# Optimization experiments

Hardware: AMD Instinct MI355X
Metric: run time of the kernel (lower is better)

Reference implementation:

```python
import jax, jax.numpy as jnp
import numpy as np

EPS = 1e-5
B, N, K = 8, 4096, 20
C_FEAT = 64            # feature channels (C_in)
HEADS, DIM_K, DIM_V = 8, 32, 16   # C_out=128 -> dim_v = 128//8
CH = 64                # ch_raise
C_CAT = 2 * C_FEAT + DIM_V        # 144, concat channel dim
C_OUT = HEADS * DIM_V


def setup_inputs() -> dict:
    key = jax.random.key(0)
    ks = jax.random.split(key, 8)
    s = lambda k, shape: jax.random.normal(k, shape, jnp.float32) * 0.05
    return {
        "x": jax.random.normal(ks[0], (B, N, 3 + C_FEAT), jnp.float32),
        "W1": s(ks[1], (CH, C_CAT)), "g1": jnp.ones(CH), "b1": jnp.zeros(CH),
        "W2": s(ks[2], (CH, CH)),    "g2": jnp.ones(CH), "b2": jnp.zeros(CH),
        "Wv": s(ks[3], (DIM_V, C_CAT)), "gv": jnp.ones(DIM_V), "bv": jnp.zeros(DIM_V),
        "Wk": s(ks[4], (DIM_K, C_CAT)),
        "Wq": s(ks[5], (HEADS * DIM_K, CH)), "gq": jnp.ones(HEADS * DIM_K), "bq": jnp.zeros(HEADS * DIM_K),
        "Wh": s(ks[6], (DIM_V, 3)),
    }


def _bn(t, g, b):
    # BatchNorm (train-mode batch stats, biased var) over all axes but channel (last)
    axes = tuple(range(t.ndim - 1))
    mu = t.mean(axes, keepdims=True)
    var = t.var(axes, keepdims=True)
    return (t - mu) * jax.lax.rsqrt(var + EPS) * g + b


def reference(x, W1, g1, b1, W2, g2, b2, Wv, gv, bv, Wk, Wq, gq, bq, Wh):
    xyz = x[..., :3]                         # [B,N,3]
    feat = x[..., 3:]                        # [B,N,C_FEAT]
    # KNN via squared distances (same formula as square_distance)
    sq = jnp.sum(xyz * xyz, -1)              # [B,N]
    d = sq[:, :, None] + sq[:, None, :] - 2.0 * jnp.einsum('bnc,bmc->bnm', xyz, xyz)
    _, idx = jax.lax.top_k(-d, K)            # smallest K -> [B,N,K]
    bi = jnp.arange(B)[:, None, None]
    nb_xyz = xyz[bi, idx]                    # [B,N,K,3]
    nb_feat = feat[bi, idx]                  # [B,N,K,C_FEAT]
    gpn = nb_feat - feat[:, :, None, :]      # grouped_points_norm
    rel = nb_xyz - xyz[:, :, None, :]        # relative positions
    pos = jnp.einsum('vc,bnkc->bnkv', Wh, rel)   # mlp_h (1x1 conv)
    fcat = jnp.concatenate(
        [gpn, jnp.broadcast_to(feat[:, :, None, :], (B, N, K, C_FEAT)), pos], -1)  # [B,N,K,C_CAT]
    # mlp: two 1x1 conv + BN + ReLU, then max over K
    h = jax.nn.relu(_bn(jnp.einsum('oc,bnkc->bnko', W1, fcat), g1, b1))
    h = jax.nn.relu(_bn(jnp.einsum('oc,bnkc->bnko', W2, h), g2, b2))
    fq = h.max(2)                            # [B,N,CH]
    q = jax.nn.relu(_bn(jnp.einsum('oc,bnc->bno', Wq, fq), gq, bq))   # [B,N,H*DK]
    q = q.reshape(B, N, HEADS, DIM_K).transpose(0, 2, 3, 1)           # b h d n
    v = _bn(jnp.einsum('vc,bnkc->bnkv', Wv, fcat), gv, bv)            # [B,N,K,DIM_V]
    kk = jax.nn.softmax(jnp.einsum('dc,bnkc->bnkd', Wk, fcat), axis=2)  # softmax over K
    kv = jnp.einsum('bnkd,bnkv->bdvn', kk, v)                         # [B,DK,DV,N]
    out = jnp.einsum('bhdn,bdvn->bhvn', q, kv)                        # [B,H,DV,N]
    out = out.reshape(B, C_OUT, N)                                    # b (h v) n
    return (xyz, out)
```

## Files before the change

### kernel.cpp

```cpp
#include <hip/hip_runtime.h>
#include <hip/hip_bf16.h>

#define NB 8
#define NN 4096
#define KK 20
#define CFEAT 64
#define CCAT 144
#define CHN 64
#define NHEAD 8
#define DKK 32
#define DVV 16
#define NQC 256
#define EPSV 1e-5f
#define BNTOT (NB*NN)
#define ITEMS (BNTOT*KK)

typedef unsigned short ushort_t;
typedef __attribute__((ext_vector_type(8))) short bf16x8;
typedef __attribute__((ext_vector_type(4))) float f32x4;


__device__ __forceinline__ float wred(float v) {
#pragma unroll
  for (int off = 32; off > 0; off >>= 1) v += __shfl_down(v, off);
  return v;
}

__device__ __forceinline__ ushort_t f2bf(float f) {
  unsigned u = __float_as_uint(f);
  return (ushort_t)((u + 0x7fffu + ((u >> 16) & 1u)) >> 16);
}
__device__ __forceinline__ float bf2f(ushort_t h) {
  return __uint_as_float(((unsigned)h) << 16);
}

__device__ __forceinline__ float pdist(float4 me, float4 p) {
  float dot = fmaf(me.x, p.x, fmaf(me.y, p.y, me.z * p.z));
  return fmaf(-2.f, dot, me.w + p.w);
}

__device__ __forceinline__ void insert20(float* bd, float d) {
#pragma unroll
  for (int j = KK - 1; j >= 1; --j)
    bd[j] = __builtin_amdgcn_fmed3f(d, bd[j - 1], bd[j]);
  bd[0] = fminf(bd[0], d);
}

__device__ __forceinline__ void build_chunk(int ch,
    const float* __restrict__ fme, const float* __restrict__ fnb,
    float rx, float ry, float rz, const float* __restrict__ Wh, float* fc)
{
  if (ch < 4) {
    int c0 = ch * 16;
#pragma unroll
    for (int j = 0; j < 16; j += 4) {
      float4 a = *(const float4*)(fnb + c0 + j);
      float4 m = *(const float4*)(fme + c0 + j);
      fc[j + 0] = a.x - m.x; fc[j + 1] = a.y - m.y;
      fc[j + 2] = a.z - m.z; fc[j + 3] = a.w - m.w;
    }
  } else if (ch < 8) {
    int c0 = (ch - 4) * 16;
#pragma unroll
    for (int j = 0; j < 16; j += 4) {
      float4 m = *(const float4*)(fme + c0 + j);
      fc[j + 0] = m.x; fc[j + 1] = m.y; fc[j + 2] = m.z; fc[j + 3] = m.w;
    }
  } else {
#pragma unroll
    for (int v = 0; v < 16; ++v)
      fc[v] = fmaf(Wh[v * 3], rx, fmaf(Wh[v * 3 + 1], ry, Wh[v * 3 + 2] * rz));
  }
}

template<int NO>
__device__ __forceinline__ void accum_chunk(const float* __restrict__ W, int ch,
                                            const float* fc, float* acc)
{
  const float* wb = W + ch * 16;
#pragma unroll
  for (int o = 0; o < NO; ++o) {
    const float* w = wb + o * CCAT;
#pragma unroll
    for (int j = 0; j < 16; ++j) acc[o] = fmaf(w[j], fc[j], acc[o]);
  }
}


__global__ void __launch_bounds__(256) k_prep(const float* __restrict__ x,
                                              float4* __restrict__ xyz4,
                                              float* __restrict__ feat,
                                              float* __restrict__ outp)
{
  __shared__ float lx[256 * 67];
  int t = threadIdx.x;
  size_t base = (size_t)blockIdx.x * 256;
  const float* xb = x + base * 67;
#pragma unroll 4
  for (int j = t; j < 256 * 67; j += 256) lx[j] = xb[j];
  __syncthreads();
  {
    float a = lx[t * 67], b = lx[t * 67 + 1], c = lx[t * 67 + 2];
    xyz4[base + t] = make_float4(a, b, c, a * a + b * b + c * c);
  }
#pragma unroll
  for (int r = 0; r < 3; ++r) {
    int j = r * 256 + t;
    outp[base * 3 + j] = lx[(j / 3) * 67 + (j % 3)];
  }
#pragma unroll 8
  for (int j = t; j < 256 * 64; j += 256)
    feat[base * 64 + j] = lx[(j >> 6) * 67 + 3 + (j & 63)];
}

#define KNQ 64
#define KNS 12
__global__ void __launch_bounds__(768) k_knn(const float4* __restrict__ xyz4,
                                             int* __restrict__ idxb)
{
  __shared__ float sbd[KNS][KNQ][21];
  __shared__ float stau[KNQ];
  __shared__ int   scnt[KNQ];
  __shared__ int   stcnt[KNQ];
  __shared__ int   sties[KNQ * 16];
  int t = threadIdx.x;
  int q = t & 63, s = t >> 6;
  int b = blockIdx.x >> 6;
  int n = ((blockIdx.x & 63) << 6) + q;
  const float4* pts = xyz4 + (size_t)b * NN;
  float4 me = pts[n];
  if (t < KNQ) { scnt[t] = 0; stcnt[t] = 0; }
  int m_lo = (s * NN) / KNS;
  int m_hi = ((s + 1) * NN) / KNS;
  int m4e = m_lo + ((m_hi - m_lo) & ~3);
  float bd[KK];
#pragma unroll
  for (int j = 0; j < KK; ++j) bd[j] = 3.4e38f;
  float4 pc0 = pts[m_lo], pc1 = pts[m_lo + 1], pc2 = pts[m_lo + 2], pc3 = pts[m_lo + 3];
#pragma unroll 1
  for (int m = m_lo; m < m4e; m += 4) {
    float4 pn0 = pts[m + 4], pn1 = pts[m + 5], pn2 = pts[m + 6], pn3 = pts[m + 7];
    float d0 = pdist(me, pc0);
    float d1 = pdist(me, pc1);
    float d2 = pdist(me, pc2);
    float d3 = pdist(me, pc3);
    insert20(bd, d0);
    insert20(bd, d1);
    insert20(bd, d2);
    insert20(bd, d3);
    pc0 = pn0; pc1 = pn1; pc2 = pn2; pc3 = pn3;
  }
#pragma unroll 1
  for (int m = m4e; m < m_hi; ++m) {
    float d = pdist(me, pts[m]);
    insert20(bd, d);
  }
#pragma unroll
  for (int j = 0; j < KK; ++j) sbd[s][q][j] = bd[j];
  sbd[s][q][KK] = 3.4e38f;
  __syncthreads();
  if (t < KNQ) {
    int ia[KNS];
#pragma unroll
    for (int ss = 0; ss < KNS; ++ss) ia[ss] = 0;
    float tau = 0.f;
#pragma unroll 1
    for (int r = 0; r < KK; ++r) {
      float best = 3.5e38f; int bs = 0;
#pragma unroll
      for (int ss = 0; ss < KNS; ++ss) {
        float v = sbd[ss][t][ia[ss]];
        if (v < best) { best = v; bs = ss; }
      }
      ia[bs]++;
      tau = best;
    }
    stau[t] = tau;
  }
  __syncthreads();
  float tau = stau[q];
  size_t obase = ((size_t)b * NN + n) * KK;
#pragma unroll 2
  for (int m = m_lo; m < m_hi; ++m) {
    float4 p = pts[m];
    float d = pdist(me, p);
    if (d < tau) {
      int slot = atomicAdd(&scnt[q], 1);
      idxb[obase + slot] = m;
    } else if (d == tau) {
      int ts_ = atomicAdd(&stcnt[q], 1);
      if (ts_ < 16) sties[q * 16 + ts_] = m;
    }
  }
  __syncthreads();
  if (t < KNQ) {
    int c1 = scnt[t];
    int tc = min(stcnt[t], 16);
    int need = KK - c1;
    size_t ob = ((size_t)b * NN + (((blockIdx.x & 63) << 6) + t)) * KK;
    int last = -1;
#pragma unroll 1
    for (int r = 0; r < need; ++r) {
      int best = 0x7fffffff;
      for (int u = 0; u < tc; ++u) {
        int mv = sties[t * 16 + u];
        if (mv > last && mv < best) best = mv;
      }
      if (best == 0x7fffffff) best = 0;
      idxb[ob + c1 + r] = best;
      last = best;
    }
  }
}

__global__ void k_red1(const float* __restrict__ st1, const float* __restrict__ g1,
                       const float* __restrict__ b1, const float* __restrict__ gv,
                       const float* __restrict__ bv, float* __restrict__ par)
{
  int o = threadIdx.x;
  const float inv = 1.f / (float)ITEMS;
  if (o < 64) {
    float s = 0.f, s2 = 0.f;
    for (int j = 0; j < 64; ++j) { s += st1[j * 160 + o]; s2 += st1[j * 160 + 64 + o]; }
    float mu = s * inv, var = s2 * inv - mu * mu;
    float a = g1[o] * rsqrtf(var + EPSV);
    par[o] = a; par[64 + o] = b1[o] - mu * a;
  } else if (o < 80) {
    int v = o - 64;
    float s = 0.f, s2 = 0.f;
    for (int j = 0; j < 64; ++j) { s += st1[j * 160 + 128 + v]; s2 += st1[j * 160 + 144 + v]; }
    float mu = s * inv, var = s2 * inv - mu * mu;
    float a = gv[v] * rsqrtf(var + EPSV);
    par[128 + v] = a; par[144 + v] = bv[v] - mu * a;
  }
}

__global__ void k_red2(const float* __restrict__ st2, const float* __restrict__ g2,
                       const float* __restrict__ b2, float* __restrict__ par)
{
  int o = threadIdx.x;
  float s = 0.f, s2 = 0.f;
  for (int j = 0; j < 64; ++j) { s += st2[j * 128 + o]; s2 += st2[j * 128 + 64 + o]; }
  const float inv = 1.f / (float)ITEMS;
  float mu = s * inv, var = s2 * inv - mu * mu;
  float a = g2[o] * rsqrtf(var + EPSV);
  par[160 + o] = a; par[224 + o] = b2[o] - mu * a;
}


__global__ void __launch_bounds__(256, 2) k_g1(
    const float4* __restrict__ xyz4, const float* __restrict__ feat,
    const int* __restrict__ idxb, const float* __restrict__ W1,
    const float* __restrict__ Wv, const float* __restrict__ Wk,
    const float* __restrict__ Wh, float* __restrict__ st1,
    ushort_t* __restrict__ t1g, ushort_t* __restrict__ akg,
    ushort_t* __restrict__ tvg)
{
  __shared__ ushort_t lds[4][16][120];
  int tid = threadIdx.x;
  int w = tid >> 6, lane = tid & 63;
  int m = lane & 15, quad = lane >> 4;

  bf16x8 Bf[7][5];
#pragma unroll
  for (int nt = 0; nt < 7; ++nt) {
    const float* wrow = (nt < 4) ? (W1 + (nt * 16 + m) * CCAT)
                      : (nt == 4) ? (Wv + m * CCAT)
                      : (Wk + ((nt - 5) * 16 + m) * CCAT);
#pragma unroll
    for (int ks = 0; ks < 5; ++ks) {
      int c0 = ks * 32 + quad * 8;
      bf16x8 f;
      if (c0 < 144) {
        float4 u = *(const float4*)(wrow + c0);
        float4 v = *(const float4*)(wrow + c0 + 4);
        f[0] = (short)f2bf(u.x); f[1] = (short)f2bf(u.y);
        f[2] = (short)f2bf(u.z); f[3] = (short)f2bf(u.w);
        f[4] = (short)f2bf(v.x); f[5] = (short)f2bf(v.y);
        f[6] = (short)f2bf(v.z); f[7] = (short)f2bf(v.w);
      } else {
#pragma unroll
        for (int j = 0; j < 8; ++j) f[j] = 0;
      }
      Bf[nt][ks] = f;
    }
  }

  float ss[5], sq[5];
#pragma unroll
  for (int i = 0; i < 5; ++i) { ss[i] = 0.f; sq[i] = 0.f; }

#pragma unroll 1
  for (int t = 0; t < 4; ++t) {
    int tile = blockIdx.x * 16 + w * 4 + t;
    int item = tile * 16 + m;
    int bn = item / 20;
    int b = bn >> 12;
    int nb = idxb[item];
    const float* fme = feat + (size_t)bn * CFEAT;
    const float* fnb = feat + ((size_t)b * NN + nb) * CFEAT;
    float4 pm = xyz4[bn];
    float4 pn = xyz4[(size_t)b * NN + nb];
    float rx = pn.x - pm.x, ry = pn.y - pm.y, rz = pn.z - pm.z;

    f32x4 acc[7];
#pragma unroll
    for (int nt = 0; nt < 7; ++nt)
#pragma unroll
      for (int r = 0; r < 4; ++r) acc[nt][r] = 0.f;

#pragma unroll
    for (int ks = 0; ks < 5; ++ks) {
      int c0 = ks * 32 + quad * 8;
      bf16x8 A;
      if (c0 < 64) {
        float4 a0 = *(const float4*)(fnb + c0);
        float4 a1 = *(const float4*)(fnb + c0 + 4);
        float4 m0 = *(const float4*)(fme + c0);
        float4 m1 = *(const float4*)(fme + c0 + 4);
        A[0] = (short)f2bf(a0.x - m0.x); A[1] = (short)f2bf(a0.y - m0.y);
        A[2] = (short)f2bf(a0.z - m0.z); A[3] = (short)f2bf(a0.w - m0.w);
        A[4] = (short)f2bf(a1.x - m1.x); A[5] = (short)f2bf(a1.y - m1.y);
        A[6] = (short)f2bf(a1.z - m1.z); A[7] = (short)f2bf(a1.w - m1.w);
      } else if (c0 < 128) {
        int c = c0 - 64;
        float4 m0 = *(const float4*)(fme + c);
        float4 m1 = *(const float4*)(fme + c + 4);
        A[0] = (short)f2bf(m0.x); A[1] = (short)f2bf(m0.y);
        A[2] = (short)f2bf(m0.z); A[3] = (short)f2bf(m0.w);
        A[4] = (short)f2bf(m1.x); A[5] = (short)f2bf(m1.y);
        A[6] = (short)f2bf(m1.z); A[7] = (short)f2bf(m1.w);
      } else if (c0 < 144) {
        int v0 = c0 - 128;
#pragma unroll
        for (int j = 0; j < 8; ++j) {
          float pv = fmaf(Wh[(v0 + j) * 3], rx,
                     fmaf(Wh[(v0 + j) * 3 + 1], ry, Wh[(v0 + j) * 3 + 2] * rz));
          A[j] = (short)f2bf(pv);
        }
      } else {
#pragma unroll
        for (int j = 0; j < 8; ++j) A[j] = 0;
      }
#pragma unroll
      for (int nt = 0; nt < 7; ++nt)
        acc[nt] = __builtin_amdgcn_mfma_f32_16x16x32_bf16(A, Bf[nt][ks], acc[nt], 0, 0, 0);
    }

#pragma unroll
    for (int nt = 0; nt < 5; ++nt)
#pragma unroll
      for (int r = 0; r < 4; ++r) {
        float v = acc[nt][r];
        ss[nt] += v; sq[nt] += v * v;
      }

#pragma unroll
    for (int nt = 0; nt < 7; ++nt)
#pragma unroll
      for (int r = 0; r < 4; ++r)
        lds[w][quad * 4 + r][nt * 16 + m] = f2bf(acc[nt][r]);
    __syncthreads();

    {
      int it = lane >> 2, sg = lane & 3;
      const uint4* sp = (const uint4*)&lds[w][it][sg * 16];
      uint4 d0 = sp[0], d1 = sp[1];
      *(uint4*)(t1g + (size_t)tile * 1024 + lane * 16) = d0;
      *(uint4*)(t1g + (size_t)tile * 1024 + lane * 16 + 8) = d1;
      const uint4* spk = (const uint4*)&lds[w][it][80 + sg * 8];
      *(uint4*)(akg + (size_t)tile * 512 + lane * 8) = spk[0];
      if (lane < 32) {
        const uint4* spv = (const uint4*)&lds[w][lane >> 1][64 + (lane & 1) * 8];
        *(uint4*)(tvg + (size_t)tile * 256 + lane * 8) = spv[0];
      }
    }
    __syncthreads();
  }

  float* slot = st1 + (blockIdx.x & 63) * 160;
#pragma unroll
  for (int nt = 0; nt < 5; ++nt) {
    float s = ss[nt];
    s += __shfl_xor(s, 16); s += __shfl_xor(s, 32);
    float q = sq[nt];
    q += __shfl_xor(q, 16); q += __shfl_xor(q, 32);
    if (lane < 16) {
      if (nt < 4) {
        atomicAdd(&slot[nt * 16 + lane], s);
        atomicAdd(&slot[64 + nt * 16 + lane], q);
      } else {
        atomicAdd(&slot[128 + lane], s);
        atomicAdd(&slot[144 + lane], q);
      }
    }
  }
}

__global__ void __launch_bounds__(256) k_g2(
    const ushort_t* __restrict__ t1g, const float* __restrict__ W2,
    const float* __restrict__ par, float* __restrict__ st2,
    float* __restrict__ fqpre)
{
  __shared__ ushort_t lds[4][80][68];
  int tid = threadIdx.x;
  int w = tid >> 6, lane = tid & 63;
  int m = lane & 15, quad = lane >> 4;
  int gw = blockIdx.x * 4 + w;

  bf16x8 Bf[4][2];
#pragma unroll
  for (int nt = 0; nt < 4; ++nt) {
    const float* wrow = W2 + (nt * 16 + m) * CHN;
#pragma unroll
    for (int ks = 0; ks < 2; ++ks) {
      int c0 = ks * 32 + quad * 8;
      float4 u = *(const float4*)(wrow + c0);
      float4 v = *(const float4*)(wrow + c0 + 4);
      bf16x8 f;
      f[0] = (short)f2bf(u.x); f[1] = (short)f2bf(u.y);
      f[2] = (short)f2bf(u.z); f[3] = (short)f2bf(u.w);
      f[4] = (short)f2bf(v.x); f[5] = (short)f2bf(v.y);
      f[6] = (short)f2bf(v.z); f[7] = (short)f2bf(v.w);
      Bf[nt][ks] = f;
    }
  }
  float pa[2][8], pb[2][8];
#pragma unroll
  for (int ks = 0; ks < 2; ++ks) {
    int c0 = ks * 32 + quad * 8;
    float4 a0 = *(const float4*)(par + c0);
    float4 a1 = *(const float4*)(par + c0 + 4);
    float4 b0 = *(const float4*)(par + 64 + c0);
    float4 b1 = *(const float4*)(par + 64 + c0 + 4);
    pa[ks][0] = a0.x; pa[ks][1] = a0.y; pa[ks][2] = a0.z; pa[ks][3] = a0.w;
    pa[ks][4] = a1.x; pa[ks][5] = a1.y; pa[ks][6] = a1.z; pa[ks][7] = a1.w;
    pb[ks][0] = b0.x; pb[ks][1] = b0.y; pb[ks][2] = b0.z; pb[ks][3] = b0.w;
    pb[ks][4] = b1.x; pb[ks][5] = b1.y; pb[ks][6] = b1.z; pb[ks][7] = b1.w;
  }

  float ss[4] = {0.f, 0.f, 0.f, 0.f}, sq[4] = {0.f, 0.f, 0.f, 0.f};

#pragma unroll 1
  for (int t5 = 0; t5 < 5; ++t5) {
    int tile = gw * 5 + t5;
    int item = tile * 16 + m;
    f32x4 acc[4];
#pragma unroll
    for (int nt = 0; nt < 4; ++nt)
#pragma unroll
      for (int r = 0; r < 4; ++r) acc[nt][r] = 0.f;
#pragma unroll
    for (int ks = 0; ks < 2; ++ks) {
      const ushort_t* tp = t1g + (size_t)item * 64 + ks * 32 + quad * 8;
      uint4 raw = *(const uint4*)tp;
      unsigned rw[4] = {raw.x, raw.y, raw.z, raw.w};
      bf16x8 A;
#pragma unroll
      for (int i = 0; i < 4; ++i) {
        float lo = bf2f((ushort_t)(rw[i] & 0xffffu));
        float hi = bf2f((ushort_t)(rw[i] >> 16));
        float h0 = fmaxf(fmaf(lo, pa[ks][2 * i], pb[ks][2 * i]), 0.f);
        float h1 = fmaxf(fmaf(hi, pa[ks][2 * i + 1], pb[ks][2 * i + 1]), 0.f);
        A[2 * i] = (short)f2bf(h0);
        A[2 * i + 1] = (short)f2bf(h1);
      }
#pragma unroll
      for (int nt = 0; nt < 4; ++nt)
        acc[nt] = __builtin_amdgcn_mfma_f32_16x16x32_bf16(A, Bf[nt][ks], acc[nt], 0, 0, 0);
    }
#pragma unroll
    for (int nt = 0; nt < 4; ++nt)
#pragma unroll
      for (int r = 0; r < 4; ++r) {
        float v = acc[nt][r];
        ss[nt] += v; sq[nt] += v * v;
        lds[w][t5 * 16 + quad * 4 + r][nt * 16 + m] = f2bf(v);
      }
  }
  __syncthreads();

  {
    int bnl = lane >> 4;
    int chb = (lane & 15) * 4;
    float mx0 = -3.4e38f, mx1 = -3.4e38f, mx2 = -3.4e38f, mx3 = -3.4e38f;
    float mn0 = 3.4e38f, mn1 = 3.4e38f, mn2 = 3.4e38f, mn3 = 3.4e38f;
#pragma unroll
    for (int j = 0; j < KK; ++j) {
      const uint2 rv = *(const uint2*)&lds[w][bnl * 20 + j][chb];
      float v0 = bf2f((ushort_t)(rv.x & 0xffffu));
      float v1 = bf2f((ushort_t)(rv.x >> 16));
      float v2 = bf2f((ushort_t)(rv.y & 0xffffu));
      float v3 = bf2f((ushort_t)(rv.y >> 16));
      mx0 = fmaxf(mx0, v0); mn0 = fminf(mn0, v0);
      mx1 = fmaxf(mx1, v1); mn1 = fminf(mn1, v1);
      mx2 = fmaxf(mx2, v2); mn2 = fminf(mn2, v2);
      mx3 = fmaxf(mx3, v3); mn3 = fminf(mn3, v3);
    }
    int bn = gw * 4 + bnl;
    *(float4*)(fqpre + (size_t)bn * 128 + chb) = make_float4(mx0, mx1, mx2, mx3);
    *(float4*)(fqpre + (size_t)bn * 128 + 64 + chb) = make_float4(mn0, mn1, mn2, mn3);
  }

  float* slot = st2 + (blockIdx.x & 63) * 128;
#pragma unroll
  for (int nt = 0; nt < 4; ++nt) {
    float s = ss[nt];
    s += __shfl_xor(s, 16); s += __shfl_xor(s, 32);
    float q = sq[nt];
    q += __shfl_xor(q, 16); q += __shfl_xor(q, 32);
    if (lane < 16) {
      atomicAdd(&slot[nt * 16 + lane], s);
      atomicAdd(&slot[64 + nt * 16 + lane], q);
    }
  }
}

#define P3P 16
__global__ void __launch_bounds__(320, 2) k_p3s(
    const ushort_t* __restrict__ akg, const ushort_t* __restrict__ tvg,
    const float* __restrict__ par, __hip_bfloat16* __restrict__ kvg)
{
  __shared__ float sl[P3P][KK][DKK + 1];
  __shared__ float sv[P3P][KK][DVV + 1];
  __shared__ float sm[P3P][DKK], ssi[P3P][DKK];
  int tid = threadIdx.x;
  int p = tid / KK, k = tid - p * KK;
  size_t item = (size_t)(blockIdx.x * P3P + p) * KK + k;
  const unsigned* ap = (const unsigned*)(akg + item * DKK);
#pragma unroll
  for (int i = 0; i < DKK / 2; ++i) {
    unsigned wv = ap[i];
    sl[p][k][2 * i]     = __uint_as_float(wv << 16);
    sl[p][k][2 * i + 1] = __uint_as_float(wv & 0xffff0000u);
  }
  const unsigned* vp = (const unsigned*)(tvg + item * DVV);
#pragma unroll
  for (int i = 0; i < DVV / 2; ++i) {
    unsigned wv = vp[i];
    float lo = __uint_as_float(wv << 16);
    float hi = __uint_as_float(wv & 0xffff0000u);
    sv[p][k][2 * i]     = fmaf(lo, par[128 + 2 * i],     par[144 + 2 * i]);
    sv[p][k][2 * i + 1] = fmaf(hi, par[128 + 2 * i + 1], par[144 + 2 * i + 1]);
  }
  __syncthreads();
  for (int pd = tid; pd < P3P * DKK; pd += 320) {
    int pp = pd >> 5, d = pd & 31;
    float m = -1e30f;
#pragma unroll
    for (int q = 0; q < KK; ++q) m = fmaxf(m, sl[pp][q][d]);
    float S = 0.f;
#pragma unroll
    for (int q = 0; q < KK; ++q) S += __expf(sl[pp][q][d] - m);
    sm[pp][d] = m; ssi[pp][d] = 1.f / S;
  }
  __syncthreads();
  for (int pd = tid; pd < P3P * DKK; pd += 320) {
    int pp = pd >> 5, d = pd & 31;
    float m = sm[pp][d], Si = ssi[pp][d];
    float a[DVV];
#pragma unroll
    for (int v = 0; v < DVV; ++v) a[v] = 0.f;
#pragma unroll
    for (int q = 0; q < KK; ++q) {
      float wgt = __expf(sl[pp][q][d] - m) * Si;
#pragma unroll
      for (int v = 0; v < DVV; ++v) a[v] = fmaf(wgt, sv[pp][q][v], a[v]);
    }
    __hip_bfloat162* dst = (__hip_bfloat162*)
        (kvg + ((size_t)(blockIdx.x * P3P + pp) * DKK + d) * DVV);
#pragma unroll
    for (int v = 0; v < DVV; v += 2) {
      float2 f2; f2.x = a[v]; f2.y = a[v + 1];
      dst[v >> 1] = __float22bfloat162_rn(f2);
    }
  }
}

__global__ void __launch_bounds__(256) k_gq(
    const float* __restrict__ fqpre, const float* __restrict__ Wq,
    const float* __restrict__ par, float* __restrict__ stq,
    float* __restrict__ q2g)
{
  int tid = threadIdx.x;
  int w = tid >> 6, lane = tid & 63;
  int m = lane & 15, quad = lane >> 4;
  int nt0 = (w & 1) * 8;
  int mt = blockIdx.x * 2 + (w >> 1);

  bf16x8 Bf[8][2];
#pragma unroll
  for (int nt = 0; nt < 8; ++nt) {
    const float* wrow = Wq + ((nt0 + nt) * 16 + m) * CHN;
#pragma unroll
    for (int ks = 0; ks < 2; ++ks) {
      int c0 = ks * 32 + quad * 8;
      float4 u = *(const float4*)(wrow + c0);
      float4 v = *(const float4*)(wrow + c0 + 4);
      bf16x8 f;
      f[0] = (short)f2bf(u.x); f[1] = (short)f2bf(u.y);
      f[2] = (short)f2bf(u.z); f[3] = (short)f2bf(u.w);
      f[4] = (short)f2bf(v.x); f[5] = (short)f2bf(v.y);
      f[6] = (short)f2bf(v.z); f[7] = (short)f2bf(v.w);
      Bf[nt][ks] = f;
    }
  }

  f32x4 acc[8];
#pragma unroll
  for (int nt = 0; nt < 8; ++nt)
#pragma unroll
    for (int r = 0; r < 4; ++r) acc[nt][r] = 0.f;

  int item = mt * 16 + m;
  const float* fp = fqpre + (size_t)item * 128;
#pragma unroll
  for (int ks = 0; ks < 2; ++ks) {
    int c0 = ks * 32 + quad * 8;
    float mxv[8], mnv[8], av[8], bv[8];
    *(float4*)&mxv[0] = *(const float4*)(fp + c0);
    *(float4*)&mxv[4] = *(const float4*)(fp + c0 + 4);
    *(float4*)&mnv[0] = *(const float4*)(fp + 64 + c0);
    *(float4*)&mnv[4] = *(const float4*)(fp + 64 + c0 + 4);
    *(float4*)&av[0] = *(const float4*)(par + 160 + c0);
    *(float4*)&av[4] = *(const float4*)(par + 160 + c0 + 4);
    *(float4*)&bv[0] = *(const float4*)(par + 224 + c0);
    *(float4*)&bv[4] = *(const float4*)(par + 224 + c0 + 4);
    bf16x8 A;
#pragma unroll
    for (int j = 0; j < 8; ++j) {
      float pick = (av[j] >= 0.f) ? mxv[j] : mnv[j];
      float fq = fmaxf(fmaf(av[j], pick, bv[j]), 0.f);
      A[j] = (short)f2bf(fq);
    }
#pragma unroll
    for (int nt = 0; nt < 8; ++nt)
      acc[nt] = __builtin_amdgcn_mfma_f32_16x16x32_bf16(A, Bf[nt][ks], acc[nt], 0, 0, 0);
  }

  float* slot = stq + (blockIdx.x & 63) * 512;
#pragma unroll
  for (int nt = 0; nt < 8; ++nt) {
    int o = (nt0 + nt) * 16 + m;
    float s = 0.f, q = 0.f;
#pragma unroll
    for (int r = 0; r < 4; ++r) {
      float v = acc[nt][r];
      q2g[(size_t)(mt * 16 + quad * 4 + r) * NQC + o] = v;
      s += v; q += v * v;
    }
    s += __shfl_xor(s, 16); s += __shfl_xor(s, 32);
    q += __shfl_xor(q, 16); q += __shfl_xor(q, 32);
    if (lane < 16) {
      atomicAdd(&slot[(nt0 + nt) * 16 + lane], s);
      atomicAdd(&slot[256 + (nt0 + nt) * 16 + lane], q);
    }
  }
}

__global__ void k_redq(const float* __restrict__ stq, const float* __restrict__ gq,
                       const float* __restrict__ bq, float* __restrict__ par)
{
  int o = threadIdx.x;
  float s = 0.f, s2 = 0.f;
  for (int j = 0; j < 64; ++j) { s += stq[j * 512 + o]; s2 += stq[j * 512 + 256 + o]; }
  const float inv = 1.f / (float)BNTOT;
  float mu = s * inv, var = s2 * inv - mu * mu;
  float a = gq[o] * rsqrtf(var + EPSV);
  par[288 + o] = a; par[544 + o] = bq[o] - mu * a;
}

__global__ void __launch_bounds__(256) k_p4(const float* __restrict__ q2g,
                                            const __hip_bfloat16* __restrict__ kvg,
                                            const float* __restrict__ par,
                                            float* __restrict__ outp)
{
  __shared__ float sq2[NQC][33];
  __shared__ unsigned skv[NQC][33];
  int t = threadIdx.x;
  int b = blockIdx.x >> 7, nc = blockIdx.x & 127;
  int bn0 = (b << 12) | (nc << 5);
#pragma unroll 4
  for (int i = t; i < 32 * NQC; i += 256) {
    int n = i >> 8, o = i & 255;
    float q = q2g[(size_t)(bn0 + n) * NQC + o];
    sq2[o][n] = fmaxf(fmaf(q, par[288 + o], par[544 + o]), 0.f);
  }
  const unsigned* kvp = (const unsigned*)kvg;
#pragma unroll 4
  for (int i = t; i < 32 * 256; i += 256) {
    int n = i >> 8, dv2 = i & 255;
    skv[dv2][n] = kvp[(size_t)(bn0 + n) * 256 + dv2];
  }
  __syncthreads();
  int n = t & 31, h = t >> 5;
  float qr[DKK];
#pragma unroll
  for (int d = 0; d < DKK; ++d) qr[d] = sq2[h * DKK + d][n];
  int n_out = (nc << 5) + n;
  size_t ob = (size_t)BNTOT * 3 + (size_t)(b * 128 + h * 16) * NN + n_out;
#pragma unroll
  for (int vv = 0; vv < DVV; vv += 2) {
    float a0 = 0.f, a1 = 0.f;
#pragma unroll
    for (int d = 0; d < DKK; ++d) {
      unsigned pk = skv[(d * DVV + vv) >> 1][n];
      a0 = fmaf(qr[d], bf2f((ushort_t)(pk & 0xffffu)), a0);
      a1 = fmaf(qr[d], bf2f((ushort_t)(pk >> 16)), a1);
    }
    outp[ob + (size_t)vv * NN] = a0;
    outp[ob + (size_t)(vv + 1) * NN] = a1;
  }
}


__global__ void __launch_bounds__(256, 3) k_s1f(
    const float4* __restrict__ xyz4, const float* __restrict__ feat,
    const int* __restrict__ idxb, const float* __restrict__ W1,
    const float* __restrict__ Wv, const float* __restrict__ Wh,
    float* __restrict__ st1,
    __hip_bfloat16* __restrict__ t1g, __hip_bfloat16* __restrict__ tvg)
{
  int t = blockIdx.x * 256 + threadIdx.x;
  int bn = t / KK, k = t - bn * KK, b = bn >> 12;
  int nb = idxb[(size_t)bn * KK + k];
  const float* fme = feat + (size_t)bn * CFEAT;
  const float* fnb = feat + ((size_t)b * NN + nb) * CFEAT;
  float4 pn = xyz4[(size_t)b * NN + nb];
  float4 pm = xyz4[bn];
  float rx = pn.x - pm.x, ry = pn.y - pm.y, rz = pn.z - pm.z;
  float a1[CHN], av[DVV];
#pragma unroll
  for (int o = 0; o < CHN; ++o) a1[o] = 0.f;
#pragma unroll
  for (int o = 0; o < DVV; ++o) av[o] = 0.f;
#pragma unroll 1
  for (int ch = 0; ch < 9; ++ch) {
    float fc[16];
    build_chunk(ch, fme, fnb, rx, ry, rz, Wh, fc);
    accum_chunk<CHN>(W1, ch, fc, a1);
    accum_chunk<DVV>(Wv, ch, fc, av);
  }
  __hip_bfloat162* t1p = (__hip_bfloat162*)(t1g + (size_t)t * CHN);
#pragma unroll
  for (int o = 0; o < CHN; o += 2) {
    float2 f2; f2.x = a1[o]; f2.y = a1[o + 1];
    t1p[o >> 1] = __float22bfloat162_rn(f2);
  }
  __hip_bfloat162* tvp = (__hip_bfloat162*)(tvg + (size_t)t * DVV);
#pragma unroll
  for (int o = 0; o < DVV; o += 2) {
    float2 f2; f2.x = av[o]; f2.y = av[o + 1];
    tvp[o >> 1] = __float22bfloat162_rn(f2);
  }
  float* slot = st1 + (blockIdx.x & 63) * 160;
  int lane = threadIdx.x & 63;
#pragma unroll
  for (int o = 0; o < CHN; ++o) {
    float s = wred(a1[o]), s2 = wred(a1[o] * a1[o]);
    if (lane == 0) { atomicAdd(&slot[o], s); atomicAdd(&slot[CHN + o], s2); }
  }
#pragma unroll
  for (int o = 0; o < DVV; ++o) {
    float s = wred(av[o]), s2 = wred(av[o] * av[o]);
    if (lane == 0) { atomicAdd(&slot[128 + o], s); atomicAdd(&slot[128 + DVV + o], s2); }
  }
}

__global__ void __launch_bounds__(256, 4) k_skf(
    const float4* __restrict__ xyz4, const float* __restrict__ feat,
    const int* __restrict__ idxb, const float* __restrict__ Wk,
    const float* __restrict__ Wh, __hip_bfloat16* __restrict__ akg)
{
  int t = blockIdx.x * 256 + threadIdx.x;
  int bn = t / KK, k = t - bn * KK, b = bn >> 12;
  int nb = idxb[(size_t)bn * KK + k];
  const float* fme = feat + (size_t)bn * CFEAT;
  const float* fnb = feat + ((size_t)b * NN + nb) * CFEAT;
  float4 pn = xyz4[(size_t)b * NN + nb];
  float4 pm = xyz4[bn];
  float rx = pn.x - pm.x, ry = pn.y - pm.y, rz = pn.z - pm.z;
  float ak[DKK];
#pragma unroll
  for (int o = 0; o < DKK; ++o) ak[o] = 0.f;
#pragma unroll 1
  for (int ch = 0; ch < 9; ++ch) {
    float fc[16];
    build_chunk(ch, fme, fnb, rx, ry, rz, Wh, fc);
    accum_chunk<DKK>(Wk, ch, fc, ak);
  }
  __hip_bfloat162* akp = (__hip_bfloat162*)(akg + (size_t)t * DKK);
#pragma unroll
  for (int o = 0; o < DKK; o += 2) {
    float2 f2; f2.x = ak[o]; f2.y = ak[o + 1];
    akp[o >> 1] = __float22bfloat162_rn(f2);
  }
}

__global__ void __launch_bounds__(256, 4) k_s2f(
    const __hip_bfloat16* __restrict__ t1g, const float* __restrict__ W2,
    const float* __restrict__ par, float* __restrict__ st2)
{
  int t = blockIdx.x * 256 + threadIdx.x;
  const unsigned* tp = (const unsigned*)(t1g + (size_t)t * CHN);
  float h1[CHN];
#pragma unroll
  for (int i = 0; i < CHN / 2; ++i) {
    unsigned w = tp[i];
    float lo = __uint_as_float(w << 16);
    float hi = __uint_as_float(w & 0xffff0000u);
    h1[2 * i]     = fmaxf(fmaf(lo, par[2 * i],     par[64 + 2 * i]),     0.f);
    h1[2 * i + 1] = fmaxf(fmaf(hi, par[2 * i + 1], par[64 + 2 * i + 1]), 0.f);
  }
  float* slot = st2 + (blockIdx.x & 63) * 128;
  int lane = threadIdx.x & 63;
#pragma unroll 1
  for (int o = 0; o < CHN; ++o) {
    const float* w = W2 + o * CHN;
    float c0 = 0.f, c1 = 0.f, c2 = 0.f, c3 = 0.f;
#pragma unroll
    for (int c = 0; c < CHN; c += 4) {
      c0 = fmaf(w[c + 0], h1[c + 0], c0); c1 = fmaf(w[c + 1], h1[c + 1], c1);
      c2 = fmaf(w[c + 2], h1[c + 2], c2); c3 = fmaf(w[c + 3], h1[c + 3], c3);
    }
    float v = (c0 + c1) + (c2 + c3);
    float s = wred(v), s2 = wred(v * v);
    if (lane == 0) { atomicAdd(&slot[o], s); atomicAdd(&slot[64 + o], s2); }
  }
}

__global__ void __launch_bounds__(320, 2) k_p3f(
    const __hip_bfloat16* __restrict__ t1g, const __hip_bfloat16* __restrict__ akg,
    const __hip_bfloat16* __restrict__ tvg, const float* __restrict__ W2,
    const float* __restrict__ par, float* __restrict__ fqg,
    __hip_bfloat16* __restrict__ kvg)
{
  __shared__ float sl[P3P][KK][DKK + 1];
  __shared__ float sv[P3P][KK][DVV + 1];
  __shared__ unsigned sfq[P3P][CHN];
  __shared__ float sm[P3P][DKK], ssi[P3P][DKK];
  int tid = threadIdx.x;
  for (int i = tid; i < P3P * CHN; i += 320) ((unsigned*)sfq)[i] = 0u;
  __syncthreads();
  int p = tid / KK, k = tid - p * KK;
  size_t item = (size_t)(blockIdx.x * P3P + p) * KK + k;
  const unsigned* ap = (const unsigned*)(akg + item * DKK);
#pragma unroll
  for (int i = 0; i < DKK / 2; ++i) {
    unsigned w = ap[i];
    sl[p][k][2 * i]     = __uint_as_float(w << 16);
    sl[p][k][2 * i + 1] = __uint_as_float(w & 0xffff0000u);
  }
  const unsigned* vp = (const unsigned*)(tvg + item * DVV);
#pragma unroll
  for (int i = 0; i < DVV / 2; ++i) {
    unsigned w = vp[i];
    float lo = __uint_as_float(w << 16);
    float hi = __uint_as_float(w & 0xffff0000u);
    sv[p][k][2 * i]     = fmaf(lo, par[128 + 2 * i],     par[144 + 2 * i]);
    sv[p][k][2 * i + 1] = fmaf(hi, par[128 + 2 * i + 1], par[144 + 2 * i + 1]);
  }
  const unsigned* tp = (const unsigned*)(t1g + item * CHN);
  float h1[CHN];
#pragma unroll
  for (int i = 0; i < CHN / 2; ++i) {
    unsigned w = tp[i];
    float lo = __uint_as_float(w << 16);
    float hi = __uint_as_float(w & 0xffff0000u);
    h1[2 * i]     = fmaxf(fmaf(lo, par[2 * i],     par[64 + 2 * i]),     0.f);
    h1[2 * i + 1] = fmaxf(fmaf(hi, par[2 * i + 1], par[64 + 2 * i + 1]), 0.f);
  }
#pragma unroll 1
  for (int o = 0; o < CHN; ++o) {
    const float* w = W2 + o * CHN;
    float c0 = 0.f, c1 = 0.f, c2 = 0.f, c3 = 0.f;
#pragma unroll
    for (int c = 0; c < CHN; c += 4) {
      c0 = fmaf(w[c + 0], h1[c + 0], c0); c1 = fmaf(w[c + 1], h1[c + 1], c1);
      c2 = fmaf(w[c + 2], h1[c + 2], c2); c3 = fmaf(w[c + 3], h1[c + 3], c3);
    }
    float v = (c0 + c1) + (c2 + c3);
    float h2 = fmaxf(fmaf(v, par[160 + o], par[224 + o]), 0.f);
    atomicMax(&sfq[p][o], __float_as_uint(h2));
  }
  __syncthreads();
  for (int i = tid; i < P3P * CHN; i += 320)
    fqg[(size_t)blockIdx.x * (P3P * CHN) + i] = __uint_as_float(sfq[i >> 6][i & 63]);
  for (int pd = tid; pd < P3P * DKK; pd += 320) {
    int pp = pd >> 5, d = pd & 31;
    float m = -1e30f;
#pragma unroll
    for (int q = 0; q < KK; ++q) m = fmaxf(m, sl[pp][q][d]);
    float S = 0.f;
#pragma unroll
    for (int q = 0; q < KK; ++q) S += __expf(sl[pp][q][d] - m);
    sm[pp][d] = m; ssi[pp][d] = 1.f / S;
  }
  __syncthreads();
  for (int pd = tid; pd < P3P * DKK; pd += 320) {
    int pp = pd >> 5, d = pd & 31;
    float m = sm[pp][d], Si = ssi[pp][d];
    float a[DVV];
#pragma unroll
    for (int v = 0; v < DVV; ++v) a[v] = 0.f;
#pragma unroll
    for (int q = 0; q < KK; ++q) {
      float wgt = __expf(sl[pp][q][d] - m) * Si;
#pragma unroll
      for (int v = 0; v < DVV; ++v) a[v] = fmaf(wgt, sv[pp][q][v], a[v]);
    }
    __hip_bfloat162* dst = (__hip_bfloat162*)
        (kvg + ((size_t)(blockIdx.x * P3P + pp) * DKK + d) * DVV);
#pragma unroll
    for (int v = 0; v < DVV; v += 2) {
      float2 f2; f2.x = a[v]; f2.y = a[v + 1];
      dst[v >> 1] = __float22bfloat162_rn(f2);
    }
  }
}

__global__ void __launch_bounds__(128, 2) k_pqf(const float* __restrict__ fqg,
                                                const float* __restrict__ Wq,
                                                float* __restrict__ stq,
                                                float* __restrict__ q2g)
{
  int bn = blockIdx.x * 128 + threadIdx.x;
  float fq[CHN];
#pragma unroll
  for (int c = 0; c < CHN; c += 4) {
    float4 v4 = *(const float4*)(fqg + (size_t)bn * CHN + c);
    fq[c] = v4.x; fq[c + 1] = v4.y; fq[c + 2] = v4.z; fq[c + 3] = v4.w;
  }
  float* slot = stq + (blockIdx.x & 63) * 512;
  int lane = threadIdx.x & 63;
#pragma unroll 1
  for (int o = 0; o < NQC; ++o) {
    const float* w = Wq + o * CHN;
    float a0 = 0.f, a1 = 0.f, a2 = 0.f, a3 = 0.f;
#pragma unroll
    for (int c = 0; c < CHN; c += 4) {
      a0 = fmaf(w[c], fq[c], a0); a1 = fmaf(w[c + 1], fq[c + 1], a1);
      a2 = fmaf(w[c + 2], fq[c + 2], a2); a3 = fmaf(w[c + 3], fq[c + 3], a3);
    }
    float v = (a0 + a1) + (a2 + a3);
    q2g[(size_t)bn * NQC + o] = v;
    float s = wred(v), s2 = wred(v * v);
    if (lane == 0) { atomicAdd(&slot[o], s); atomicAdd(&slot[256 + o], s2); }
  }
}

__global__ void __launch_bounds__(64) k_p4f(const float* __restrict__ q2g,
                                            const __hip_bfloat16* __restrict__ kvg,
                                            const float* __restrict__ par,
                                            float* __restrict__ outp)
{
  __shared__ float sq2[NQC], skv[DKK * DVV];
  int t = threadIdx.x;
  int b = blockIdx.x & 7, n = blockIdx.x >> 3;
  int bn = (b << 12) | n;
#pragma unroll
  for (int j = 0; j < 8; ++j)
    skv[t + 64 * j] = __bfloat162float(kvg[(size_t)bn * 512 + t + 64 * j]);
#pragma unroll
  for (int j = 0; j < 4; ++j) {
    int o = t + 64 * j;
    float v = q2g[(size_t)bn * NQC + o];
    sq2[o] = fmaxf(fmaf(v, par[288 + o], par[544 + o]), 0.f);
  }
  __syncthreads();
#pragma unroll
  for (int j = 0; j < 2; ++j) {
    int ch = t + 64 * j, h = ch >> 4, vv = ch & 15;
    float a = 0.f;
#pragma unroll
    for (int d = 0; d < DKK; ++d) a = fmaf(sq2[h * DKK + d], skv[d * DVV + vv], a);
    outp[(size_t)BNTOT * 3 + ((size_t)(b * 128 + ch)) * NN + n] = a;
  }
}


extern "C" void kernel_launch(void* const* d_in, const int* in_sizes, int n_in,
                              void* d_out, int out_size, void* d_ws, size_t ws_size,
                              hipStream_t stream)
{
  const float* x  = (const float*)d_in[0];
  const float* W1 = (const float*)d_in[1];
  const float* g1 = (const float*)d_in[2];
  const float* b1 = (const float*)d_in[3];
  const float* W2 = (const float*)d_in[4];
  const float* g2 = (const float*)d_in[5];
  const float* b2 = (const float*)d_in[6];
  const float* Wv = (const float*)d_in[7];
  const float* gv = (const float*)d_in[8];
  const float* bv = (const float*)d_in[9];
  const float* Wk = (const float*)d_in[10];
  const float* Wq = (const float*)d_in[11];
  const float* gq = (const float*)d_in[12];
  const float* bq = (const float*)d_in[13];
  const float* Wh = (const float*)d_in[14];

  float* ws = (float*)d_ws;
  float4* xyz4 = (float4*)ws;
  float*  feat = ws + 131072;
  int*    idxb = (int*)(ws + 2228224);
  float*  st1  = ws + 2883584;
  float*  st2  = ws + 2893824;
  float*  stq  = ws + 2902016;
  float*  par  = ws + 2934784;
  float*  fqg  = ws + 2935584;
  __hip_bfloat16* kvg = (__hip_bfloat16*)(ws + 5032736);
  float*  outp = (float*)d_out;

  ushort_t* t1g = (ushort_t*)(ws + 13421344);
  ushort_t* akg = (ushort_t*)(ws + 34392864);
  ushort_t* tvg = (ushort_t*)(ws + 44878624);
  float*    fqpre = ws + 50121504;
  float*    q2g = ws + 13421344;

  const size_t NEW_NEED  = (size_t)54315808 * 4;

  hipMemsetAsync(st1, 0, (size_t)(10240 + 8192 + 32768) * sizeof(float), stream);
  k_prep<<<128, 256, 0, stream>>>(x, xyz4, feat, outp);
  k_knn <<<512, 768, 0, stream>>>(xyz4, idxb);

  if (ws_size >= NEW_NEED) {
    k_g1  <<<2560, 256, 0, stream>>>(xyz4, feat, idxb, W1, Wv, Wk, Wh, st1, t1g, akg, tvg);
    k_red1<<<1, 128, 0, stream>>>(st1, g1, b1, gv, bv, par);
    k_g2  <<<2048, 256, 0, stream>>>(t1g, W2, par, st2, fqpre);
    k_red2<<<1, 64, 0, stream>>>(st2, g2, b2, par);
    k_p3s <<<2048, 320, 0, stream>>>(akg, tvg, par, kvg);
    k_gq  <<<1024, 256, 0, stream>>>(fqpre, Wq, par, stq, q2g);
    k_redq<<<1, 256, 0, stream>>>(stq, gq, bq, par);
    k_p4  <<<1024, 256, 0, stream>>>(q2g, kvg, par, outp);
  } else {
    __hip_bfloat16* t1b = (__hip_bfloat16*)t1g;
    __hip_bfloat16* akb = (__hip_bfloat16*)akg;
    __hip_bfloat16* tvb = (__hip_bfloat16*)tvg;
    float* q2f = ws + 34392864;
    k_s1f <<<2560, 256, 0, stream>>>(xyz4, feat, idxb, W1, Wv, Wh, st1, t1b, tvb);
    k_skf <<<2560, 256, 0, stream>>>(xyz4, feat, idxb, Wk, Wh, akb);
    k_red1<<<1, 128, 0, stream>>>(st1, g1, b1, gv, bv, par);
    k_s2f <<<2560, 256, 0, stream>>>(t1b, W2, par, st2);
    k_red2<<<1, 64, 0, stream>>>(st2, g2, b2, par);
    k_p3f <<<2048, 320, 0, stream>>>(t1b, akb, tvb, W2, par, fqg, kvg);
    k_pqf <<<256, 128, 0, stream>>>(fqg, Wq, stq, q2f);
    k_redq<<<1, 256, 0, stream>>>(stq, gq, bq, par);
    k_p4f <<<32768, 64, 0, stream>>>(q2f, kvg, par, outp);
  }
}
```

Measured before the change: 573.6 us.

## Split KNN into four kernels with segment partial top-k and global merge

Replaces the single fused KNN kernel with a multi-pass pipeline. Each query first keeps per-segment top-20 distances for 16 segments in global memory. A merge pass then derives each query's threshold, a third pass rescans and emits indices below the threshold via global atomics, and a final pass fills remaining slots from ties. This raises the number of blocks and removes the shared-memory merge, at the cost of extra global traffic, a second full distance scan, atomics and more launches.

Result: slower. 669.4 us (+16.7%).

```diff
diff --git a/kernel.cpp b/kernel.cpp
--- a/kernel.cpp
+++ b/kernel.cpp
@@ -111,6 +111,115 @@
 #pragma unroll 8
   for (int j = t; j < 256 * 64; j += 256)
     feat[base * 64 + j] = lx[(j >> 6) * 67 + 3 + (j & 63)];
+}
+
+#define KSEG 16
+__global__ void __launch_bounds__(256) k_knn1(const float4* __restrict__ xyz4,
+                                              float* __restrict__ sbdg)
+{
+  int bi = blockIdx.x;
+  int sg = bi & 3, qg = (bi >> 2) & 63, b = bi >> 8;
+  int w = threadIdx.x >> 6, lane = threadIdx.x & 63;
+  int seg = sg * 4 + w;
+  int n = (qg << 6) + lane;
+  const float4* pts = xyz4 + (size_t)b * NN;
+  float4 me = pts[n];
+  float bd[KK];
+#pragma unroll
+  for (int j = 0; j < KK; ++j) bd[j] = 3.4e38f;
+  int m0 = seg << 8;
+  float4 pc0 = pts[m0], pc1 = pts[m0 + 1], pc2 = pts[m0 + 2], pc3 = pts[m0 + 3];
+#pragma unroll 1
+  for (int m = m0; m < m0 + 256; m += 4) {
+    float4 pn0 = pts[m + 4], pn1 = pts[m + 5], pn2 = pts[m + 6], pn3 = pts[m + 7];
+    float d0 = pdist(me, pc0);
+    float d1 = pdist(me, pc1);
+    float d2 = pdist(me, pc2);
+    float d3 = pdist(me, pc3);
+    insert20(bd, d0);
+    insert20(bd, d1);
+    insert20(bd, d2);
+    insert20(bd, d3);
+    pc0 = pn0; pc1 = pn1; pc2 = pn2; pc3 = pn3;
+  }
+  float* dst = sbdg + ((size_t)(b * NN + n) * KSEG + seg) * KK;
+#pragma unroll
+  for (int j = 0; j < KK; ++j) dst[j] = bd[j];
+}
+
+__global__ void __launch_bounds__(256) k_knn2(const float* __restrict__ sbdg,
+                                              float* __restrict__ taug)
+{
+  int bn = blockIdx.x * 256 + threadIdx.x;
+  const float* base = sbdg + (size_t)bn * (KSEG * KK);
+  float bd[KK];
+#pragma unroll
+  for (int j = 0; j < KK; ++j) bd[j] = 3.4e38f;
+#pragma unroll 1
+  for (int m = 0; m < KSEG * KK; m += 4) {
+    float4 v = *(const float4*)(base + m);
+    insert20(bd, v.x);
+    insert20(bd, v.y);
+    insert20(bd, v.z);
+    insert20(bd, v.w);
+  }
+  taug[bn] = bd[19];
+}
+
+__global__ void __launch_bounds__(256) k_knn3(const float4* __restrict__ xyz4,
+                                              const float* __restrict__ taug,
+                                              int* __restrict__ idxb,
+                                              int* __restrict__ gscnt,
+                                              int* __restrict__ gstcnt,
+                                              int* __restrict__ gsties)
+{
+  int bi = blockIdx.x;
+  int sg = bi & 3, qg = (bi >> 2) & 63, b = bi >> 8;
+  int w = threadIdx.x >> 6, lane = threadIdx.x & 63;
+  int seg = sg * 4 + w;
+  int n = (qg << 6) + lane;
+  int bn = b * NN + n;
+  const float4* pts = xyz4 + (size_t)b * NN;
+  float4 me = pts[n];
+  float tau = taug[bn];
+  size_t obase = (size_t)bn * KK;
+  int m0 = seg << 8;
+#pragma unroll 2
+  for (int m = m0; m < m0 + 256; ++m) {
+    float4 p = pts[m];
+    float d = pdist(me, p);
+    if (d < tau) {
+      int slot = atomicAdd(&gscnt[bn], 1);
+      idxb[obase + slot] = m;
+    } else if (d == tau) {
+      int ts_ = atomicAdd(&gstcnt[bn], 1);
+      if (ts_ < 16) gsties[bn * 16 + ts_] = m;
+    }
+  }
+}
+
+__global__ void __launch_bounds__(256) k_knn4(const int* __restrict__ gscnt,
+                                              const int* __restrict__ gstcnt,
+                                              const int* __restrict__ gsties,
+                                              int* __restrict__ idxb)
+{
+  int bn = blockIdx.x * 256 + threadIdx.x;
+  int c1 = gscnt[bn];
+  int tc = min(gstcnt[bn], 16);
+  int need = KK - c1;
+  size_t ob = (size_t)bn * KK;
+  int last = -1;
+#pragma unroll 1
+  for (int r = 0; r < need; ++r) {
+    int best = 0x7fffffff;
+    for (int u = 0; u < tc; ++u) {
+      int mv = gsties[bn * 16 + u];
+      if (mv > last && mv < best) best = mv;
+    }
+    if (best == 0x7fffffff) best = 0;
+    idxb[ob + c1 + r] = best;
+    last = best;
+  }
 }
 
 #define KNQ 64
@@ -1017,11 +1126,27 @@
   float*    fqpre = ws + 50121504;
   float*    q2g = ws + 13421344;
 
-  const size_t NEW_NEED  = (size_t)54315808 * 4;
+  float* sbdg  = ws + 54315808;
+  float* taug  = ws + 64801568;
+  int*   gscnt = (int*)(ws + 64834336);
+  int*   gstcnt= (int*)(ws + 64867104);
+  int*   gsties= (int*)(ws + 64899872);
+
+  const size_t NEW_NEED = (size_t)54315808 * 4;
+  const size_t KNN_NEED = (size_t)65424160 * 4;
 
   hipMemsetAsync(st1, 0, (size_t)(10240 + 8192 + 32768) * sizeof(float), stream);
   k_prep<<<128, 256, 0, stream>>>(x, xyz4, feat, outp);
-  k_knn <<<512, 768, 0, stream>>>(xyz4, idxb);
+
+  if (ws_size >= KNN_NEED) {
+    hipMemsetAsync(gscnt, 0, (size_t)65536 * sizeof(int), stream);
+    k_knn1<<<2048, 256, 0, stream>>>(xyz4, sbdg);
+    k_knn2<<<128, 256, 0, stream>>>(sbdg, taug);
+    k_knn3<<<2048, 256, 0, stream>>>(xyz4, taug, idxb, gscnt, gstcnt, gsties);
+    k_knn4<<<128, 256, 0, stream>>>(gscnt, gstcnt, gsties, idxb);
+  } else {
+    k_knn<<<512, 768, 0, stream>>>(xyz4, idxb);
+  }
 
   if (ws_size >= NEW_NEED) {
     k_g1  <<<2560, 256, 0, stream>>>(xyz4, feat, idxb, W1, Wv, Wk, Wh, st1, t1g, akg, tvg);
```
